# Kernel tuning notes

Hardware: AMD Instinct MI355X
Metric: run time of the kernel (lower is better)

Reference implementation:

```python
import jax, jax.numpy as jnp
import numpy as np

D_MODEL = 1024
D_FF = 2048
NUM_GROUPS = 4
EXPERTS_PER_GROUP = 4
TOP_K = 2
N_TOKENS = 4096
TOTAL_EXPERTS = NUM_GROUPS * EXPERTS_PER_GROUP


def setup_inputs() -> dict:
    key = jax.random.key(0)
    ks = jax.random.split(key, 7)
    s = 0.02
    return {
        "x": jax.random.normal(ks[0], (N_TOKENS, D_MODEL), dtype=jnp.float32),
        "Wg": jax.random.normal(ks[1], (D_MODEL, NUM_GROUPS), dtype=jnp.float32) * s,
        "We": jax.random.normal(ks[2], (D_MODEL, TOTAL_EXPERTS), dtype=jnp.float32) * s,
        "w1": jax.random.normal(ks[3], (TOTAL_EXPERTS, D_MODEL, D_FF), dtype=jnp.float32) * s,
        "b1": jnp.zeros((TOTAL_EXPERTS, D_FF), dtype=jnp.float32),
        "w2": jax.random.normal(ks[4], (TOTAL_EXPERTS, D_FF, D_MODEL), dtype=jnp.float32) * s,
        "b2": jnp.zeros((TOTAL_EXPERTS, D_MODEL), dtype=jnp.float32),
    }


def _router(x, Wg, We):
    N = x.shape[0]
    G, Eg = NUM_GROUPS, EXPERTS_PER_GROUP
    # Level 1: group gate
    group_probs = jax.nn.softmax(x @ Wg, axis=-1)            # [N, G]
    group_mask = group_probs >= (1.0 / G)
    # Level 2: expert gate (per-group softmax)
    expert_logits = (x @ We).reshape(N, G, Eg)
    expert_probs = jax.nn.softmax(expert_logits, axis=-1)    # [N, G, Eg]
    expert_mask = expert_probs >= (1.0 / Eg)
    valid_mask = (group_mask[:, :, None] & expert_mask).reshape(N, G * Eg)
    final_probs = (group_probs[:, :, None] * expert_probs).reshape(N, G * Eg)
    # Fallback: if fewer than top_k experts pass thresholds, use top-k by prob
    num_selected = valid_mask.sum(axis=-1)
    _, topk_idx = jax.lax.top_k(final_probs, TOP_K)          # [N, top_k]
    topk_mask = jnp.zeros((N, G * Eg), dtype=bool).at[
        jnp.arange(N)[:, None], topk_idx].set(True)
    use_topk = num_selected < TOP_K
    final_mask = jnp.where(use_topk[:, None], topk_mask, valid_mask)
    sel = final_probs * final_mask.astype(final_probs.dtype)
    w = sel / jnp.clip(sel.sum(axis=-1, keepdims=True), 1e-9)
    return final_mask, w                                      # [N, E], [N, E]


def reference(x, Wg, We, w1, b1, w2, b2):
    _, weights = _router(x, Wg, We)                          # [N, E]
    # Dense expert compute; masked-out experts contribute weight 0,
    # matching the gather/FFN/index_add loop in the original.
    h = jax.nn.gelu(jnp.einsum("nd,edf->nef", x, w1) + b1, approximate=False)
    y = jnp.einsum("nef,efd->ned", h, w2) + b2               # [N, E, D]
    return jnp.einsum("ne,ned->nd", weights, y)              # [N, D]
```

## Files before the change

kernel.cpp:

```cpp
#include <hip/hip_runtime.h>
#include <math.h>

#define NT 4096
#define DM 1024
#define DF 2048
#define NEXP 16

typedef __attribute__((ext_vector_type(8))) short bf16x8;
typedef __attribute__((ext_vector_type(4))) float f32x4;

__device__ __forceinline__ unsigned short f2bf(float f) {
  unsigned int u = __builtin_bit_cast(unsigned int, f);
  u += 0x7fffu + ((u >> 16) & 1u);
  return (unsigned short)(u >> 16);
}
__device__ __forceinline__ float bf2f(unsigned short s) {
  unsigned int u = ((unsigned int)s) << 16;
  return __builtin_bit_cast(float, u);
}

__device__ __forceinline__ void gload_lds16(const void* g, void* l) {
  __builtin_amdgcn_global_load_lds(
      (__attribute__((address_space(1))) void*)g,
      (__attribute__((address_space(3))) void*)l, 16, 0, 0);
}

__device__ __forceinline__ float gelu_f(float v) {
  float u = v * (0.7978845608f + 0.0356774081f * v * v);
  float t = 1.0f - 2.0f / (__expf(2.0f * u) + 1.0f);
  return 0.5f * v * (1.0f + t);
}

__device__ __forceinline__ void softmax4(float* v) {
  float m = fmaxf(fmaxf(v[0], v[1]), fmaxf(v[2], v[3]));
  float s = 0.f;
#pragma unroll
  for (int j = 0; j < 4; ++j) { v[j] = expf(v[j] - m); s += v[j]; }
  float inv = 1.f / s;
#pragma unroll
  for (int j = 0; j < 4; ++j) v[j] *= inv;
}

__global__ __launch_bounds__(256) void router2_kernel(
    const float* __restrict__ x, const float* __restrict__ Wg,
    const float* __restrict__ We, unsigned int* __restrict__ emask,
    float* __restrict__ eweight, unsigned short* __restrict__ xb) {
  int n = blockIdx.x;
  int tid = threadIdx.x;
  int c0 = tid * 4;
  float4 xv = *(const float4*)(x + (size_t)n * DM + c0);
  if (xb) {
    ushort4 o = make_ushort4(f2bf(xv.x), f2bf(xv.y), f2bf(xv.z), f2bf(xv.w));
    *(ushort4*)(xb + (size_t)n * DM + c0) = o;
  }
  float xa[4] = {xv.x, xv.y, xv.z, xv.w};
  float acc[20];
#pragma unroll
  for (int j = 0; j < 20; ++j) acc[j] = 0.f;
#pragma unroll
  for (int j = 0; j < 4; ++j) {
    int c = c0 + j;
    float4 wg = *(const float4*)(Wg + c * 4);
    acc[0] += xa[j] * wg.x; acc[1] += xa[j] * wg.y;
    acc[2] += xa[j] * wg.z; acc[3] += xa[j] * wg.w;
#pragma unroll
    for (int q = 0; q < 4; ++q) {
      float4 we = *(const float4*)(We + c * 16 + q * 4);
      acc[4 + q * 4 + 0] += xa[j] * we.x;
      acc[4 + q * 4 + 1] += xa[j] * we.y;
      acc[4 + q * 4 + 2] += xa[j] * we.z;
      acc[4 + q * 4 + 3] += xa[j] * we.w;
    }
  }
#pragma unroll
  for (int j = 0; j < 20; ++j) {
    float v = acc[j];
#pragma unroll
    for (int s = 32; s; s >>= 1) v += __shfl_xor(v, s, 64);
    acc[j] = v;
  }
  __shared__ float red[4][20];
  int lane = tid & 63, wv = tid >> 6;
  if (lane == 0) {
#pragma unroll
    for (int j = 0; j < 20; ++j) red[wv][j] = acc[j];
  }
  __syncthreads();
  if (tid == 0) {
    float t[20];
#pragma unroll
    for (int j = 0; j < 20; ++j)
      t[j] = red[0][j] + red[1][j] + red[2][j] + red[3][j];
    float gp[4] = {t[0], t[1], t[2], t[3]};
    softmax4(gp);
    float ep[16];
#pragma unroll
    for (int g = 0; g < 4; ++g) {
      float tt[4] = {t[4 + g * 4], t[5 + g * 4], t[6 + g * 4], t[7 + g * 4]};
      softmax4(tt);
#pragma unroll
      for (int i = 0; i < 4; ++i) ep[g * 4 + i] = tt[i];
    }
    float fp[16];
    bool valid[16];
    int nsel = 0;
#pragma unroll
    for (int g = 0; g < 4; ++g) {
      bool gm = gp[g] >= 0.25f;
#pragma unroll
      for (int i = 0; i < 4; ++i) {
        int e = g * 4 + i;
        bool em = ep[e] >= 0.25f;
        valid[e] = gm && em;
        fp[e] = gp[g] * ep[e];
        nsel += valid[e] ? 1 : 0;
      }
    }
    int m1 = 0; float v1 = -1.f;
#pragma unroll
    for (int e = 0; e < 16; ++e) if (fp[e] > v1) { v1 = fp[e]; m1 = e; }
    int m2 = -1; float v2 = -2.f;
#pragma unroll
    for (int e = 0; e < 16; ++e) if (e != m1 && fp[e] > v2) { v2 = fp[e]; m2 = e; }
    bool use_topk = nsel < 2;
    float sel[16]; float s = 0.f;
#pragma unroll
    for (int e = 0; e < 16; ++e) {
      bool msk = use_topk ? (e == m1 || e == m2) : valid[e];
      sel[e] = msk ? fp[e] : 0.f;
      s += sel[e];
      valid[e] = msk;
    }
    float inv = 1.f / fmaxf(s, 1e-9f);
    unsigned int mbits = 0;
    float wv16[16];
#pragma unroll
    for (int e = 0; e < 16; ++e) {
      mbits |= (valid[e] ? 1u : 0u) << e;
      wv16[e] = valid[e] ? sel[e] * inv : 0.f;
    }
    emask[n] = mbits;
#pragma unroll
    for (int i = 0; i < 4; ++i)
      *(float4*)(eweight + (size_t)n * 16 + i * 4) =
          make_float4(wv16[i * 4], wv16[i * 4 + 1], wv16[i * 4 + 2], wv16[i * 4 + 3]);
  }
}

__global__ __launch_bounds__(256) void compact_kernel(
    const unsigned int* __restrict__ emask, const float* __restrict__ eweight,
    int* __restrict__ counts, int* __restrict__ lists, float* __restrict__ wl,
    int* __restrict__ slotpos) {
  int e = blockIdx.x;
  int tid = threadIdx.x, lane = tid & 63, wv = tid >> 6;
  __shared__ int wcnt[4];
  int running = 0;
  for (int base = 0; base < NT; base += 256) {
    int n = base + tid;
    bool p = (emask[n] >> e) & 1u;
    unsigned long long bal = __ballot(p);
    int cnt = __popcll(bal);
    if (lane == 0) wcnt[wv] = cnt;
    __syncthreads();
    int off = running;
#pragma unroll
    for (int w = 0; w < 4; ++w)
      if (w < wv) off += wcnt[w];
    int tot = wcnt[0] + wcnt[1] + wcnt[2] + wcnt[3];
    if (p) {
      int pos = off + (int)__popcll(bal & ((1ull << lane) - 1ull));
      lists[e * NT + pos] = n;
      wl[e * NT + pos] = eweight[(size_t)n * 16 + e];
      slotpos[e * NT + n] = pos;
    }
    running += tot;
    __syncthreads();
  }
  if (tid == 0) counts[e] = running;
}

__global__ void prefix_kernel(const int* __restrict__ counts, int* __restrict__ base,
                              int* __restrict__ ent, int* __restrict__ nent) {
  if (threadIdx.x == 0 && blockIdx.x == 0) {
    int acc = 0, n = 0;
    for (int e = 0; e < NEXP; ++e) {
      base[e] = acc;
      acc += (counts[e] + 255) & ~255;
      int mt = (counts[e] + 127) >> 7;
      for (int m = 0; m < mt; ++m) ent[n++] = (e << 16) | m;
    }
    *nent = n;
  }
}

__global__ __launch_bounds__(256) void wtrans_kernel(
    const float* __restrict__ in, unsigned short* __restrict__ outp, int K, int N) {
  int e = blockIdx.z;
  int n0 = blockIdx.x * 64;
  int k0 = blockIdx.y * 64;
  const float* src = in + (size_t)e * K * N;
  unsigned short* dst = outp + (size_t)e * K * N;
  __shared__ unsigned short t[64][65];
  int tid = threadIdx.x;
#pragma unroll
  for (int it = 0; it < 4; ++it) {
    int idx = it * 256 + tid;
    int r = idx >> 4, c4 = (idx & 15) << 2;
    float4 v = *(const float4*)(src + (size_t)(k0 + r) * N + n0 + c4);
    t[r][c4 + 0] = f2bf(v.x);
    t[r][c4 + 1] = f2bf(v.y);
    t[r][c4 + 2] = f2bf(v.z);
    t[r][c4 + 3] = f2bf(v.w);
  }
  __syncthreads();
#pragma unroll
  for (int it = 0; it < 4; ++it) {
    int idx = it * 256 + tid;
    int r = idx >> 4, c4 = (idx & 15) << 2;
    ushort4 o;
    o.x = t[c4 + 0][r]; o.y = t[c4 + 1][r];
    o.z = t[c4 + 2][r]; o.w = t[c4 + 3][r];
    *(ushort4*)(dst + (size_t)(n0 + r) * K + k0 + c4) = o;
  }
}


__global__ __launch_bounds__(256, 4) void ffn1s_kernel(
    const unsigned short* __restrict__ xb, const unsigned short* __restrict__ wt,
    const float* __restrict__ b1, const int* __restrict__ counts,
    const int* __restrict__ lists, const int* __restrict__ base,
    unsigned short* __restrict__ h, int cap) {
  const int NN = DF / 128;
  const int NSLOT = 128;
  int b = blockIdx.x;
  int xcd = b & 7, slot = b >> 3;
  int e0 = xcd, e1 = xcd + 8;
  int c0 = counts[e0], c1 = counts[e1];
  int mt0 = (c0 + 127) >> 7, mt1 = (c1 + 127) >> 7;
  int T0 = mt0 * NN, T = T0 + mt1 * NN;

  __shared__ unsigned short lA[128 * 64];
  __shared__ unsigned short lB[128 * 64];

  int tid = threadIdx.x, lane = tid & 63, wid = tid >> 6;
  int wm = wid >> 1, wn = wid & 1;
  int lrow = lane & 15, lk = lane >> 4;
  int chunk = lane & 7, row_l = lane >> 3;

  for (int k = slot; k < T; k += NSLOT) {
    int e, mti, nt, count;
    if (k < T0) { e = e0; nt = k / mt0; mti = k % mt0; count = c0; }
    else        { int kk = k - T0; e = e1; nt = kk / mt1; mti = kk % mt1; count = c1; }
    int m0 = mti * 128, n0 = nt * 128;
    int hbase = base[e];
    if (hbase + m0 + 128 > cap) continue;
    const unsigned short* we = wt + (size_t)e * DM * DF;
    const int* lst = lists + e * NT + m0;

    const char* asrc[4];
    const char* bsrc[4];
#pragma unroll
    for (int c = 0; c < 4; ++c) {
      int r = wid * 32 + c * 8 + row_l;
      int sc = chunk ^ (r & 7);
      int rr = (m0 + r < count) ? r : 0;
      int tok = lst[rr];
      asrc[c] = (const char*)xb + (size_t)tok * DM * 2 + sc * 16;
      bsrc[c] = (const char*)we + (size_t)(n0 + r) * DM * 2 + sc * 16;
    }

    f32x4 acc[4][4];
#pragma unroll
    for (int m = 0; m < 4; ++m)
#pragma unroll
      for (int n = 0; n < 4; ++n) acc[m][n] = (f32x4)0.0f;

    for (int kt = 0; kt < DM / 64; ++kt) {
      __syncthreads();
#pragma unroll
      for (int c = 0; c < 4; ++c) {
        gload_lds16(asrc[c] + kt * 128, (void*)(lA + (wid * 32 + c * 8) * 64));
        gload_lds16(bsrc[c] + kt * 128, (void*)(lB + (wid * 32 + c * 8) * 64));
      }
      __syncthreads();
#pragma unroll
      for (int ks = 0; ks < 2; ++ks) {
        bf16x8 af[4], bfr[4];
#pragma unroll
        for (int m = 0; m < 4; ++m) {
          int row = wm * 64 + m * 16 + lrow;
          int off = row * 128 + (((ks * 64) + lk * 16) ^ ((row & 7) << 4));
          af[m] = *(const bf16x8*)((const char*)lA + off);
        }
#pragma unroll
        for (int n = 0; n < 4; ++n) {
          int row = wn * 64 + n * 16 + lrow;
          int off = row * 128 + (((ks * 64) + lk * 16) ^ ((row & 7) << 4));
          bfr[n] = *(const bf16x8*)((const char*)lB + off);
        }
#pragma unroll
        for (int m = 0; m < 4; ++m)
#pragma unroll
          for (int n = 0; n < 4; ++n)
            acc[m][n] = __builtin_amdgcn_mfma_f32_16x16x32_bf16(af[m], bfr[n], acc[m][n], 0, 0, 0);
      }
    }
#pragma unroll
    for (int m = 0; m < 4; ++m) {
      int rbase = hbase + m0 + wm * 64 + m * 16 + lk * 4;
#pragma unroll
      for (int n = 0; n < 4; ++n) {
        int col = n0 + wn * 64 + n * 16 + lrow;
        float bias = b1[e * DF + col];
#pragma unroll
        for (int j = 0; j < 4; ++j) {
          float v = acc[m][n][j] + bias;
          h[(size_t)(rbase + j) * DF + col] = f2bf(gelu_f(v));
        }
      }
    }
  }
}

__global__ __launch_bounds__(256, 4) void ffn2y_kernel(
    const unsigned short* __restrict__ h, const unsigned short* __restrict__ wt,
    const int* __restrict__ counts, const int* __restrict__ base,
    unsigned short* __restrict__ y, int cap) {
  const int NN = DM / 128;
  const int NSLOT = 128;
  int b = blockIdx.x;
  int xcd = b & 7, slot = b >> 3;
  int e0 = xcd, e1 = xcd + 8;
  int c0 = counts[e0], c1 = counts[e1];
  int mt0 = (c0 + 127) >> 7, mt1 = (c1 + 127) >> 7;
  int T0 = mt0 * NN, T = T0 + mt1 * NN;

  __shared__ unsigned short lA[128 * 64];
  __shared__ unsigned short lB[128 * 64];

  int tid = threadIdx.x, lane = tid & 63, wid = tid >> 6;
  int wm = wid >> 1, wn = wid & 1;
  int lrow = lane & 15, lk = lane >> 4;
  int chunk = lane & 7, row_l = lane >> 3;

  for (int k = slot; k < T; k += NSLOT) {
    int e, mti, nt, count;
    if (k < T0) { e = e0; nt = k / mt0; mti = k % mt0; count = c0; }
    else        { int kk = k - T0; e = e1; nt = kk / mt1; mti = kk % mt1; count = c1; }
    int m0 = mti * 128, n0 = nt * 128;
    int hbase = base[e];
    if (hbase + m0 + 128 > cap) continue;
    const unsigned short* we = wt + (size_t)e * DM * DF;

    const char* asrc[4];
    const char* bsrc[4];
#pragma unroll
    for (int c = 0; c < 4; ++c) {
      int r = wid * 32 + c * 8 + row_l;
      int sc = chunk ^ (r & 7);
      asrc[c] = (const char*)h + (size_t)(hbase + m0 + r) * DF * 2 + sc * 16;
      bsrc[c] = (const char*)we + (size_t)(n0 + r) * DF * 2 + sc * 16;
    }

    f32x4 acc[4][4];
#pragma unroll
    for (int m = 0; m < 4; ++m)
#pragma unroll
      for (int n = 0; n < 4; ++n) acc[m][n] = (f32x4)0.0f;

    for (int kt = 0; kt < DF / 64; ++kt) {
      __syncthreads();
#pragma unroll
      for (int c = 0; c < 4; ++c) {
        gload_lds16(asrc[c] + kt * 128, (void*)(lA + (wid * 32 + c * 8) * 64));
        gload_lds16(bsrc[c] + kt * 128, (void*)(lB + (wid * 32 + c * 8) * 64));
      }
      __syncthreads();
#pragma unroll
      for (int ks = 0; ks < 2; ++ks) {
        bf16x8 af[4], bfr[4];
#pragma unroll
        for (int m = 0; m < 4; ++m) {
          int row = wm * 64 + m * 16 + lrow;
          int off = row * 128 + (((ks * 64) + lk * 16) ^ ((row & 7) << 4));
          af[m] = *(const bf16x8*)((const char*)lA + off);
        }
#pragma unroll
        for (int n = 0; n < 4; ++n) {
          int row = wn * 64 + n * 16 + lrow;
          int off = row * 128 + (((ks * 64) + lk * 16) ^ ((row & 7) << 4));
          bfr[n] = *(const bf16x8*)((const char*)lB + off);
        }
#pragma unroll
        for (int m = 0; m < 4; ++m)
#pragma unroll
          for (int n = 0; n < 4; ++n)
            acc[m][n] = __builtin_amdgcn_mfma_f32_16x16x32_bf16(af[m], bfr[n], acc[m][n], 0, 0, 0);
      }
    }
#pragma unroll
    for (int m = 0; m < 4; ++m) {
      int rbase = hbase + m0 + wm * 64 + m * 16 + lk * 4;
      int lcl = m0 + wm * 64 + m * 16 + lk * 4;
#pragma unroll
      for (int n = 0; n < 4; ++n) {
        int col = n0 + wn * 64 + n * 16 + lrow;
#pragma unroll
        for (int j = 0; j < 4; ++j) {
          if (lcl + j < count)
            y[(size_t)(rbase + j) * DM + col] = f2bf(acc[m][n][j]);
        }
      }
    }
  }
}

__global__ __launch_bounds__(256) void reduce_kernel(
    const unsigned int* __restrict__ emask, const float* __restrict__ eweight,
    const int* __restrict__ slotpos, const int* __restrict__ base,
    const unsigned short* __restrict__ y, const float* __restrict__ b2,
    float* __restrict__ out) {
  int n = blockIdx.x;
  int tid = threadIdx.x;
  int c = tid * 4;
  unsigned int mask = emask[n];
  float4 accv = make_float4(0.f, 0.f, 0.f, 0.f);
  while (mask) {
    int e = __ffs(mask) - 1;
    mask &= mask - 1;
    float w = eweight[(size_t)n * 16 + e];
    int row = base[e] + slotpos[e * NT + n];
    ushort4 yv = *(const ushort4*)(y + (size_t)row * DM + c);
    float4 bv = *(const float4*)(b2 + e * DM + c);
    accv.x += w * (bf2f(yv.x) + bv.x);
    accv.y += w * (bf2f(yv.y) + bv.y);
    accv.z += w * (bf2f(yv.z) + bv.z);
    accv.w += w * (bf2f(yv.w) + bv.w);
  }
  *(float4*)(out + (size_t)n * DM + c) = accv;
}

__global__ __launch_bounds__(256, 4) void ffn2s_kernel(
    const unsigned short* __restrict__ h, const unsigned short* __restrict__ wt,
    const float* __restrict__ b2, const int* __restrict__ counts,
    const int* __restrict__ lists, const int* __restrict__ base,
    const float* __restrict__ wl, float* __restrict__ out, int cap) {
  const int NN = DM / 128;
  const int NSLOT = 128;
  int b = blockIdx.x;
  int xcd = b & 7, slot = b >> 3;
  int e0 = xcd, e1 = xcd + 8;
  int c0 = counts[e0], c1 = counts[e1];
  int mt0 = (c0 + 127) >> 7, mt1 = (c1 + 127) >> 7;
  int T0 = mt0 * NN, T = T0 + mt1 * NN;

  __shared__ unsigned short lA[128 * 64];
  __shared__ unsigned short lB[128 * 64];

  int tid = threadIdx.x, lane = tid & 63, wid = tid >> 6;
  int wm = wid >> 1, wn = wid & 1;
  int lrow = lane & 15, lk = lane >> 4;
  int chunk = lane & 7, row_l = lane >> 3;

  for (int k = slot; k < T; k += NSLOT) {
    int e, mti, nt, count;
    if (k < T0) { e = e0; nt = k / mt0; mti = k % mt0; count = c0; }
    else        { int kk = k - T0; e = e1; nt = kk / mt1; mti = kk % mt1; count = c1; }
    int m0 = mti * 128, n0 = nt * 128;
    int hbase = base[e];
    if (hbase + m0 + 128 > cap) continue;
    const unsigned short* we = wt + (size_t)e * DM * DF;

    const char* asrc[4];
    const char* bsrc[4];
#pragma unroll
    for (int c = 0; c < 4; ++c) {
      int r = wid * 32 + c * 8 + row_l;
      int sc = chunk ^ (r & 7);
      asrc[c] = (const char*)h + (size_t)(hbase + m0 + r) * DF * 2 + sc * 16;
      bsrc[c] = (const char*)we + (size_t)(n0 + r) * DF * 2 + sc * 16;
    }

    f32x4 acc[4][4];
#pragma unroll
    for (int m = 0; m < 4; ++m)
#pragma unroll
      for (int n = 0; n < 4; ++n) acc[m][n] = (f32x4)0.0f;

    for (int kt = 0; kt < DF / 64; ++kt) {
      __syncthreads();
#pragma unroll
      for (int c = 0; c < 4; ++c) {
        gload_lds16(asrc[c] + kt * 128, (void*)(lA + (wid * 32 + c * 8) * 64));
        gload_lds16(bsrc[c] + kt * 128, (void*)(lB + (wid * 32 + c * 8) * 64));
      }
      __syncthreads();
#pragma unroll
      for (int ks = 0; ks < 2; ++ks) {
        bf16x8 af[4], bfr[4];
#pragma unroll
        for (int m = 0; m < 4; ++m) {
          int row = wm * 64 + m * 16 + lrow;
          int off = row * 128 + (((ks * 64) + lk * 16) ^ ((row & 7) << 4));
          af[m] = *(const bf16x8*)((const char*)lA + off);
        }
#pragma unroll
        for (int n = 0; n < 4; ++n) {
          int row = wn * 64 + n * 16 + lrow;
          int off = row * 128 + (((ks * 64) + lk * 16) ^ ((row & 7) << 4));
          bfr[n] = *(const bf16x8*)((const char*)lB + off);
        }
#pragma unroll
        for (int m = 0; m < 4; ++m)
#pragma unroll
          for (int n = 0; n < 4; ++n)
            acc[m][n] = __builtin_amdgcn_mfma_f32_16x16x32_bf16(af[m], bfr[n], acc[m][n], 0, 0, 0);
      }
    }
#pragma unroll
    for (int m = 0; m < 4; ++m) {
      int rbase = m0 + wm * 64 + m * 16 + lk * 4;
#pragma unroll
      for (int n = 0; n < 4; ++n) {
        int col = n0 + wn * 64 + n * 16 + lrow;
        float bias = b2[e * DM + col];
#pragma unroll
        for (int j = 0; j < 4; ++j) {
          int sl = rbase + j;
          if (sl < count) {
            int tok = lists[e * NT + sl];
            float w = wl[e * NT + sl];
            atomicAdd(out + (size_t)tok * DM + col, w * (acc[m][n][j] + bias));
          }
        }
      }
    }
  }
}

__global__ __launch_bounds__(256) void ffn1_kernel(
    const float* __restrict__ x, const float* __restrict__ w1,
    const float* __restrict__ b1, const int* __restrict__ counts,
    const int* __restrict__ lists, const int* __restrict__ base,
    unsigned short* __restrict__ h, int cap, int e_arg) {
  int e = (e_arg >= 0) ? e_arg : (int)blockIdx.z;
  int count = counts[e];
  int m0 = blockIdx.y * 128;
  if (m0 >= count) return;
  int hbase = base[e];
  if (hbase + m0 + 128 > cap) return;
  int n0 = blockIdx.x * 128;
  const float* w1e = w1 + (size_t)e * DM * DF;
  const int* lst = lists + e * NT + m0;
  __shared__ unsigned short lA[128 * 64];
  __shared__ unsigned short lB[128 * 64];
  int tid = threadIdx.x;
  int lane = tid & 63, wid = tid >> 6;
  int wm = wid >> 1, wn = wid & 1;
  int lrow = lane & 15, lk = lane >> 4;
  f32x4 acc[4][4];
#pragma unroll
  for (int m = 0; m < 4; ++m)
#pragma unroll
    for (int n = 0; n < 4; ++n) acc[m][n] = (f32x4)0.0f;
  for (int kt = 0; kt < DM / 64; ++kt) {
    int k0 = kt * 64;
    __syncthreads();
#pragma unroll
    for (int p = 0; p < 8; ++p) {
      int idx = p * 256 + tid;
      int r = idx >> 4, c4 = idx & 15;
      int tok = (m0 + r < count) ? lst[r] : lst[0];
      float4 v = *(const float4*)(x + (size_t)tok * DM + k0 + c4 * 4);
      ushort4 bv = make_ushort4(f2bf(v.x), f2bf(v.y), f2bf(v.z), f2bf(v.w));
      int off = r * 128 + ((c4 * 8) ^ ((r & 7) << 4));
      *(ushort4*)((char*)lA + off) = bv;
    }
#pragma unroll
    for (int p = 0; p < 16; ++p) {
      int idx = p * 256 + tid;
      int n = idx & 127, k2 = idx >> 7;
      const float* bp = w1e + (size_t)(k0 + 2 * k2) * DF + n0 + n;
      ushort2 bv = make_ushort2(f2bf(bp[0]), f2bf(bp[DF]));
      int off = n * 128 + ((k2 * 4) ^ ((n & 7) << 4));
      *(ushort2*)((char*)lB + off) = bv;
    }
    __syncthreads();
#pragma unroll
    for (int ks = 0; ks < 2; ++ks) {
      bf16x8 af[4], bfr[4];
#pragma unroll
      for (int m = 0; m < 4; ++m) {
        int row = wm * 64 + m * 16 + lrow;
        int off = row * 128 + (((ks * 64) + lk * 16) ^ ((row & 7) << 4));
        af[m] = *(const bf16x8*)((const char*)lA + off);
      }
#pragma unroll
      for (int n = 0; n < 4; ++n) {
        int row = wn * 64 + n * 16 + lrow;
        int off = row * 128 + (((ks * 64) + lk * 16) ^ ((row & 7) << 4));
        bfr[n] = *(const bf16x8*)((const char*)lB + off);
      }
#pragma unroll
      for (int m = 0; m < 4; ++m)
#pragma unroll
        for (int n = 0; n < 4; ++n)
          acc[m][n] = __builtin_amdgcn_mfma_f32_16x16x32_bf16(af[m], bfr[n], acc[m][n], 0, 0, 0);
    }
  }
#pragma unroll
  for (int m = 0; m < 4; ++m) {
    int rbase = hbase + m0 + wm * 64 + m * 16 + lk * 4;
#pragma unroll
    for (int n = 0; n < 4; ++n) {
      int col = n0 + wn * 64 + n * 16 + lrow;
      float bias = b1[e * DF + col];
#pragma unroll
      for (int j = 0; j < 4; ++j) {
        float v = acc[m][n][j] + bias;
        h[(size_t)(rbase + j) * DF + col] = f2bf(gelu_f(v));
      }
    }
  }
}

__global__ __launch_bounds__(256) void ffn2_kernel(
    const unsigned short* __restrict__ h, const float* __restrict__ w2,
    const float* __restrict__ b2, const int* __restrict__ counts,
    const int* __restrict__ lists, const int* __restrict__ base,
    const float* __restrict__ wl, float* __restrict__ out, int cap, int e_arg) {
  int e = (e_arg >= 0) ? e_arg : (int)blockIdx.z;
  int count = counts[e];
  int m0 = blockIdx.y * 128;
  if (m0 >= count) return;
  int hbase = base[e];
  if (hbase + m0 + 128 > cap) return;
  int n0 = blockIdx.x * 128;
  const float* w2e = w2 + (size_t)e * DF * DM;
  __shared__ unsigned short lA[128 * 64];
  __shared__ unsigned short lB[128 * 64];
  int tid = threadIdx.x;
  int lane = tid & 63, wid = tid >> 6;
  int wm = wid >> 1, wn = wid & 1;
  int lrow = lane & 15, lk = lane >> 4;
  f32x4 acc[4][4];
#pragma unroll
  for (int m = 0; m < 4; ++m)
#pragma unroll
    for (int n = 0; n < 4; ++n) acc[m][n] = (f32x4)0.0f;
  for (int kt = 0; kt < DF / 64; ++kt) {
    int k0 = kt * 64;
    __syncthreads();
#pragma unroll
    for (int p = 0; p < 8; ++p) {
      int idx = p * 256 + tid;
      int r = idx >> 4, c4 = idx & 15;
      ushort4 v = *(const ushort4*)(h + (size_t)(hbase + m0 + r) * DF + k0 + c4 * 4);
      int off = r * 128 + ((c4 * 8) ^ ((r & 7) << 4));
      *(ushort4*)((char*)lA + off) = v;
    }
#pragma unroll
    for (int p = 0; p < 16; ++p) {
      int idx = p * 256 + tid;
      int n = idx & 127, k2 = idx >> 7;
      const float* bp = w2e + (size_t)(k0 + 2 * k2) * DM + n0 + n;
      ushort2 bv = make_ushort2(f2bf(bp[0]), f2bf(bp[DM]));
      int off = n * 128 + ((k2 * 4) ^ ((n & 7) << 4));
      *(ushort2*)((char*)lB + off) = bv;
    }
    __syncthreads();
#pragma unroll
    for (int ks = 0; ks < 2; ++ks) {
      bf16x8 af[4], bfr[4];
#pragma unroll
      for (int m = 0; m < 4; ++m) {
        int row = wm * 64 + m * 16 + lrow;
        int off = row * 128 + (((ks * 64) + lk * 16) ^ ((row & 7) << 4));
        af[m] = *(const bf16x8*)((const char*)lA + off);
      }
#pragma unroll
      for (int n = 0; n < 4; ++n) {
        int row = wn * 64 + n * 16 + lrow;
        int off = row * 128 + (((ks * 64) + lk * 16) ^ ((row & 7) << 4));
        bfr[n] = *(const bf16x8*)((const char*)lB + off);
      }
#pragma unroll
      for (int m = 0; m < 4; ++m)
#pragma unroll
        for (int n = 0; n < 4; ++n)
          acc[m][n] = __builtin_amdgcn_mfma_f32_16x16x32_bf16(af[m], bfr[n], acc[m][n], 0, 0, 0);
    }
  }
#pragma unroll
  for (int m = 0; m < 4; ++m) {
    int rbase = m0 + wm * 64 + m * 16 + lk * 4;
#pragma unroll
    for (int n = 0; n < 4; ++n) {
      int col = n0 + wn * 64 + n * 16 + lrow;
      float bias = b2[e * DM + col];
#pragma unroll
      for (int j = 0; j < 4; ++j) {
        int slot = rbase + j;
        if (slot < count) {
          int tok = lists[e * NT + slot];
          float w = wl[e * NT + slot];
          atomicAdd(out + (size_t)tok * DM + col, w * (acc[m][n][j] + bias));
        }
      }
    }
  }
}

extern "C" void kernel_launch(void* const* d_in, const int* in_sizes, int n_in,
                              void* d_out, int out_size, void* d_ws, size_t ws_size,
                              hipStream_t stream) {
  const float* x  = (const float*)d_in[0];
  const float* Wg = (const float*)d_in[1];
  const float* We = (const float*)d_in[2];
  const float* w1 = (const float*)d_in[3];
  const float* b1 = (const float*)d_in[4];
  const float* w2 = (const float*)d_in[5];
  const float* b2 = (const float*)d_in[6];
  float* out = (float*)d_out;

  char* ws = (char*)d_ws;
  int* counts = (int*)ws;
  int* base   = (int*)(ws + 256);
  int* nent   = (int*)(ws + 576);
  int* ent    = (int*)(ws + 1024);
  unsigned int* emask = (unsigned int*)(ws + 4096);
  int* lists  = (int*)(ws + 32768);
  float* wl   = (float*)(ws + 32768 + NEXP * NT * 4);
  float* eweight = (float*)(ws + 32768 + 2 * NEXP * NT * 4);
  int* slotpos   = (int*)(ws + 32768 + 3 * NEXP * NT * 4);

  const size_t OFF_XB = 2u << 20;
  const size_t OFF_WT = OFF_XB + ((size_t)NT * DM * 2);
  const size_t OFF_H  = OFF_WT + ((size_t)NEXP * DM * DF * 2);
  long cap6 = ((long)ws_size - (long)OFF_H) / (DF * 2 + DM * 2);
  long cap4 = ((long)ws_size - (long)OFF_H) / (DF * 2);
  bool fast = (cap4 >= 20000);

  unsigned short* xb_router = fast ? (unsigned short*)(ws + OFF_XB) : (unsigned short*)0;

  hipMemsetAsync(out, 0, (size_t)NT * DM * sizeof(float), stream);
  hipMemsetAsync(ws, 0, 1024, stream);
  router2_kernel<<<NT, 256, 0, stream>>>(x, Wg, We, emask, eweight, xb_router);
  compact_kernel<<<NEXP, 256, 0, stream>>>(emask, eweight, counts, lists, wl, slotpos);

  if (fast) {
    unsigned short* xb = (unsigned short*)(ws + OFF_XB);
    unsigned short* wt = (unsigned short*)(ws + OFF_WT);
    unsigned short* h  = (unsigned short*)(ws + OFF_H);
    prefix_kernel<<<1, 64, 0, stream>>>(counts, base, ent, nent);
    wtrans_kernel<<<dim3(DF / 64, DM / 64, NEXP), 256, 0, stream>>>(w1, wt, DM, DF);
    if (cap6 >= 20000) {
      int cap = (int)(cap6 > 65536 ? 65536 : cap6);
      unsigned short* y = (unsigned short*)(ws + OFF_H + (size_t)cap * DF * 2);
      ffn1s_kernel<<<1024, 256, 0, stream>>>(xb, wt, b1, counts, lists, base, h, cap);
      wtrans_kernel<<<dim3(DM / 64, DF / 64, NEXP), 256, 0, stream>>>(w2, wt, DF, DM);
      ffn2y_kernel<<<1024, 256, 0, stream>>>(h, wt, counts, base, y, cap);
      reduce_kernel<<<NT, 256, 0, stream>>>(emask, eweight, slotpos, base, y, b2, out);
    } else {
      int cap = (int)(cap4 > 65536 ? 65536 : cap4);
      ffn1s_kernel<<<1024, 256, 0, stream>>>(xb, wt, b1, counts, lists, base, h, cap);
      wtrans_kernel<<<dim3(DM / 64, DF / 64, NEXP), 256, 0, stream>>>(w2, wt, DF, DM);
      ffn2s_kernel<<<1024, 256, 0, stream>>>(h, wt, b2, counts, lists, base, wl, out, cap);
    }
  } else {
    unsigned short* h = (unsigned short*)(ws + OFF_XB);
    long cap_rows = ((long)ws_size - (long)OFF_XB) / (DF * 2);
    if (cap_rows >= 24576) {
      int cap = (int)(cap_rows > 65536 ? 65536 : cap_rows);
      prefix_kernel<<<1, 64, 0, stream>>>(counts, base, ent, nent);
      ffn1_kernel<<<dim3(DF / 128, NT / 128, NEXP), 256, 0, stream>>>(
          x, w1, b1, counts, lists, base, h, cap, -1);
      ffn2_kernel<<<dim3(DM / 128, NT / 128, NEXP), 256, 0, stream>>>(
          h, w2, b2, counts, lists, base, wl, out, cap, -1);
    } else {
      hipMemsetAsync(base, 0, 64, stream);
      for (int e = 0; e < NEXP; ++e) {
        ffn1_kernel<<<dim3(DF / 128, NT / 128, 1), 256, 0, stream>>>(
            x, w1, b1, counts, lists, base, h, NT, e);
        ffn2_kernel<<<dim3(DM / 128, NT / 128, 1), 256, 0, stream>>>(
            h, w2, b2, counts, lists, base, wl, out, NT, e);
      }
    }
  }
}
```

Baseline: 310.6 us.

## Fuse weight transposes into router and FFN1 kernels via extra blocks

Adds dedicated blocks to the router kernel that transpose and convert w1 to bf16 while other blocks compute routing, and adds blocks to the FFN1 kernel that transpose w2 into a separate buffer while FFN1 runs. This removes the standalone wtrans launches and their serialization, so conversion overlaps with compute. It needs extra workspace for a separate w2t buffer and falls back to the old sequence when workspace is short. The fallback small path now calls prefix_kernel after the base memset, which may change behavior there.

Result: no change. 314.2 us (+1.2%).

```diff
diff --git a/kernel.cpp b/kernel.cpp
--- a/kernel.cpp
+++ b/kernel.cpp
@@ -41,12 +41,52 @@
   for (int j = 0; j < 4; ++j) v[j] *= inv;
 }
 
-__global__ __launch_bounds__(256) void router2_kernel(
+__device__ __forceinline__ void trans_tile(
+    const float* __restrict__ src, unsigned short* __restrict__ dst,
+    int K, int N, int k0, int n0, unsigned short (*t)[65], int tid) {
+#pragma unroll
+  for (int it = 0; it < 4; ++it) {
+    int idx = it * 256 + tid;
+    int r = idx >> 4, c4 = (idx & 15) << 2;
+    float4 v = *(const float4*)(src + (size_t)(k0 + r) * N + n0 + c4);
+    t[r][c4 + 0] = f2bf(v.x);
+    t[r][c4 + 1] = f2bf(v.y);
+    t[r][c4 + 2] = f2bf(v.z);
+    t[r][c4 + 3] = f2bf(v.w);
+  }
+  __syncthreads();
+#pragma unroll
+  for (int it = 0; it < 4; ++it) {
+    int idx = it * 256 + tid;
+    int r = idx >> 4, c4 = (idx & 15) << 2;
+    ushort4 o;
+    o.x = t[c4 + 0][r]; o.y = t[c4 + 1][r];
+    o.z = t[c4 + 2][r]; o.w = t[c4 + 3][r];
+    *(ushort4*)(dst + (size_t)(n0 + r) * K + k0 + c4) = o;
+  }
+  __syncthreads();
+}
+
+__global__ __launch_bounds__(256) void prep1_kernel(
     const float* __restrict__ x, const float* __restrict__ Wg,
     const float* __restrict__ We, unsigned int* __restrict__ emask,
-    float* __restrict__ eweight, unsigned short* __restrict__ xb) {
-  int n = blockIdx.x;
-  int tid = threadIdx.x;
+    float* __restrict__ eweight, unsigned short* __restrict__ xb,
+    const float* __restrict__ w1, unsigned short* __restrict__ w1t, int wtB) {
+  __shared__ unsigned short tbuf[64][65];
+  __shared__ float red[4][20];
+  int id = blockIdx.x, tid = threadIdx.x;
+  if (id < wtB) {
+    int per = 8192 / wtB;
+    for (int i = 0; i < per; ++i) {
+      int t = id * per + i;
+      int e = t >> 9, rem = t & 511;
+      int n0 = (rem & 31) * 64, k0 = (rem >> 5) * 64;
+      trans_tile(w1 + (size_t)e * DM * DF, w1t + (size_t)e * DM * DF,
+                 DM, DF, k0, n0, tbuf, tid);
+    }
+    return;
+  }
+  int n = id - wtB;
   int c0 = tid * 4;
   float4 xv = *(const float4*)(x + (size_t)n * DM + c0);
   if (xb) {
@@ -79,7 +119,6 @@
     for (int s = 32; s; s >>= 1) v += __shfl_xor(v, s, 64);
     acc[j] = v;
   }
-  __shared__ float red[4][20];
   int lane = tid & 63, wv = tid >> 6;
   if (lane == 0) {
 #pragma unroll
@@ -195,54 +234,45 @@
 
 __global__ __launch_bounds__(256) void wtrans_kernel(
     const float* __restrict__ in, unsigned short* __restrict__ outp, int K, int N) {
+  __shared__ unsigned short t[64][65];
   int e = blockIdx.z;
   int n0 = blockIdx.x * 64;
   int k0 = blockIdx.y * 64;
-  const float* src = in + (size_t)e * K * N;
-  unsigned short* dst = outp + (size_t)e * K * N;
-  __shared__ unsigned short t[64][65];
-  int tid = threadIdx.x;
-#pragma unroll
-  for (int it = 0; it < 4; ++it) {
-    int idx = it * 256 + tid;
-    int r = idx >> 4, c4 = (idx & 15) << 2;
-    float4 v = *(const float4*)(src + (size_t)(k0 + r) * N + n0 + c4);
-    t[r][c4 + 0] = f2bf(v.x);
-    t[r][c4 + 1] = f2bf(v.y);
-    t[r][c4 + 2] = f2bf(v.z);
-    t[r][c4 + 3] = f2bf(v.w);
-  }
-  __syncthreads();
-#pragma unroll
-  for (int it = 0; it < 4; ++it) {
-    int idx = it * 256 + tid;
-    int r = idx >> 4, c4 = (idx & 15) << 2;
-    ushort4 o;
-    o.x = t[c4 + 0][r]; o.y = t[c4 + 1][r];
-    o.z = t[c4 + 2][r]; o.w = t[c4 + 3][r];
-    *(ushort4*)(dst + (size_t)(n0 + r) * K + k0 + c4) = o;
-  }
-}
-
-
-__global__ __launch_bounds__(256, 4) void ffn1s_kernel(
+  trans_tile(in + (size_t)e * K * N, outp + (size_t)e * K * N, K, N, k0, n0, t,
+             threadIdx.x);
+}
+
+__global__ __launch_bounds__(256, 4) void ffn1h_kernel(
     const unsigned short* __restrict__ xb, const unsigned short* __restrict__ wt,
     const float* __restrict__ b1, const int* __restrict__ counts,
     const int* __restrict__ lists, const int* __restrict__ base,
-    unsigned short* __restrict__ h, int cap) {
+    unsigned short* __restrict__ h, int cap,
+    const float* __restrict__ w2, unsigned short* __restrict__ w2t, int wtB) {
+  __shared__ unsigned short lA[128 * 64];
+  __shared__ unsigned short lB[128 * 64];
+  int id = blockIdx.x, tid = threadIdx.x;
+  if (id < wtB) {
+    unsigned short(*tbuf)[65] = (unsigned short(*)[65])lA;
+    int per = 8192 / wtB;
+    for (int i = 0; i < per; ++i) {
+      int t = id * per + i;
+      int e = t >> 9, rem = t & 511;
+      int n0 = (rem & 15) * 64, k0 = (rem >> 4) * 64;
+      trans_tile(w2 + (size_t)e * DF * DM, w2t + (size_t)e * DF * DM,
+                 DF, DM, k0, n0, tbuf, tid);
+    }
+    return;
+  }
+  int g = id - wtB;
   const int NN = DF / 128;
   const int NSLOT = 128;
-  int b = blockIdx.x;
-  int xcd = b & 7, slot = b >> 3;
+  int xcd = g & 7, slot = g >> 3;
   int e0 = xcd, e1 = xcd + 8;
   int c0 = counts[e0], c1 = counts[e1];
   int mt0 = (c0 + 127) >> 7, mt1 = (c1 + 127) >> 7;
   int T0 = mt0 * NN, T = T0 + mt1 * NN;
 
-  __shared__ unsigned short lA[128 * 64];
-  __shared__ unsigned short lB[128 * 64];
-
-  int tid = threadIdx.x, lane = tid & 63, wid = tid >> 6;
+  int lane = tid & 63, wid = tid >> 6;
   int wm = wid >> 1, wn = wid & 1;
   int lrow = lane & 15, lk = lane >> 4;
   int chunk = lane & 7, row_l = lane >> 3;
@@ -734,40 +764,62 @@
   float* eweight = (float*)(ws + 32768 + 2 * NEXP * NT * 4);
   int* slotpos   = (int*)(ws + 32768 + 3 * NEXP * NT * 4);
 
-  const size_t OFF_XB = 2u << 20;
-  const size_t OFF_WT = OFF_XB + ((size_t)NT * DM * 2);
-  const size_t OFF_H  = OFF_WT + ((size_t)NEXP * DM * DF * 2);
-  long cap6 = ((long)ws_size - (long)OFF_H) / (DF * 2 + DM * 2);
-  long cap4 = ((long)ws_size - (long)OFF_H) / (DF * 2);
-  bool fast = (cap4 >= 20000);
-
-  unsigned short* xb_router = fast ? (unsigned short*)(ws + OFF_XB) : (unsigned short*)0;
+  const size_t OFF_XB  = (size_t)2 << 20;
+  const size_t OFF_W1T = OFF_XB + ((size_t)NT * DM * 2);
+  const size_t WTSZ    = (size_t)NEXP * DM * DF * 2;
+  const size_t OFF_W2T = OFF_W1T + WTSZ;
+  const size_t OFF_H_A = OFF_W2T + WTSZ;
+  const size_t OFF_H_B = OFF_W1T + WTSZ;
+
+  long capA = ((long)ws_size - (long)OFF_H_A) / ((DF + DM) * 2);
+  long capB = ((long)ws_size - (long)OFF_H_B) / ((DF + DM) * 2);
+  long capC = ((long)ws_size - (long)OFF_H_B) / (DF * 2);
+  bool fast = (capC >= 20000);
+
+  unsigned short* xb = (unsigned short*)(ws + OFF_XB);
+  unsigned short* w1t = (unsigned short*)(ws + OFF_W1T);
 
   hipMemsetAsync(out, 0, (size_t)NT * DM * sizeof(float), stream);
   hipMemsetAsync(ws, 0, 1024, stream);
-  router2_kernel<<<NT, 256, 0, stream>>>(x, Wg, We, emask, eweight, xb_router);
-  compact_kernel<<<NEXP, 256, 0, stream>>>(emask, eweight, counts, lists, wl, slotpos);
 
   if (fast) {
-    unsigned short* xb = (unsigned short*)(ws + OFF_XB);
-    unsigned short* wt = (unsigned short*)(ws + OFF_WT);
-    unsigned short* h  = (unsigned short*)(ws + OFF_H);
+    prep1_kernel<<<1024 + NT, 256, 0, stream>>>(x, Wg, We, emask, eweight, xb,
+                                                w1, w1t, 1024);
+    compact_kernel<<<NEXP, 256, 0, stream>>>(emask, eweight, counts, lists, wl, slotpos);
     prefix_kernel<<<1, 64, 0, stream>>>(counts, base, ent, nent);
-    wtrans_kernel<<<dim3(DF / 64, DM / 64, NEXP), 256, 0, stream>>>(w1, wt, DM, DF);
-    if (cap6 >= 20000) {
-      int cap = (int)(cap6 > 65536 ? 65536 : cap6);
-      unsigned short* y = (unsigned short*)(ws + OFF_H + (size_t)cap * DF * 2);
-      ffn1s_kernel<<<1024, 256, 0, stream>>>(xb, wt, b1, counts, lists, base, h, cap);
-      wtrans_kernel<<<dim3(DM / 64, DF / 64, NEXP), 256, 0, stream>>>(w2, wt, DF, DM);
-      ffn2y_kernel<<<1024, 256, 0, stream>>>(h, wt, counts, base, y, cap);
+
+    if (capA >= 20000) {
+      int cap = (int)(capA > 65536 ? 65536 : capA);
+      unsigned short* w2t = (unsigned short*)(ws + OFF_W2T);
+      unsigned short* h = (unsigned short*)(ws + OFF_H_A);
+      unsigned short* y = (unsigned short*)(ws + OFF_H_A + (size_t)cap * DF * 2);
+      ffn1h_kernel<<<512 + 1024, 256, 0, stream>>>(
+          xb, w1t, b1, counts, lists, base, h, cap, w2, w2t, 512);
+      ffn2y_kernel<<<1024, 256, 0, stream>>>(h, w2t, counts, base, y, cap);
+      reduce_kernel<<<NT, 256, 0, stream>>>(emask, eweight, slotpos, base, y, b2, out);
+    } else if (capB >= 20000) {
+      int cap = (int)(capB > 65536 ? 65536 : capB);
+      unsigned short* h = (unsigned short*)(ws + OFF_H_B);
+      unsigned short* y = (unsigned short*)(ws + OFF_H_B + (size_t)cap * DF * 2);
+      ffn1h_kernel<<<1024, 256, 0, stream>>>(
+          xb, w1t, b1, counts, lists, base, h, cap, (const float*)0,
+          (unsigned short*)0, 0);
+      wtrans_kernel<<<dim3(DM / 64, DF / 64, NEXP), 256, 0, stream>>>(w2, w1t, DF, DM);
+      ffn2y_kernel<<<1024, 256, 0, stream>>>(h, w1t, counts, base, y, cap);
       reduce_kernel<<<NT, 256, 0, stream>>>(emask, eweight, slotpos, base, y, b2, out);
     } else {
-      int cap = (int)(cap4 > 65536 ? 65536 : cap4);
-      ffn1s_kernel<<<1024, 256, 0, stream>>>(xb, wt, b1, counts, lists, base, h, cap);
-      wtrans_kernel<<<dim3(DM / 64, DF / 64, NEXP), 256, 0, stream>>>(w2, wt, DF, DM);
-      ffn2s_kernel<<<1024, 256, 0, stream>>>(h, wt, b2, counts, lists, base, wl, out, cap);
+      int cap = (int)(capC > 65536 ? 65536 : capC);
+      unsigned short* h = (unsigned short*)(ws + OFF_H_B);
+      ffn1h_kernel<<<1024, 256, 0, stream>>>(
+          xb, w1t, b1, counts, lists, base, h, cap, (const float*)0,
+          (unsigned short*)0, 0);
+      wtrans_kernel<<<dim3(DM / 64, DF / 64, NEXP), 256, 0, stream>>>(w2, w1t, DF, DM);
+      ffn2s_kernel<<<1024, 256, 0, stream>>>(h, w1t, b2, counts, lists, base, wl, out, cap);
     }
   } else {
+    prep1_kernel<<<NT, 256, 0, stream>>>(x, Wg, We, emask, eweight,
+                                         (unsigned short*)0, w1, w1t, 0);
+    compact_kernel<<<NEXP, 256, 0, stream>>>(emask, eweight, counts, lists, wl, slotpos);
     unsigned short* h = (unsigned short*)(ws + OFF_XB);
     long cap_rows = ((long)ws_size - (long)OFF_XB) / (DF * 2);
     if (cap_rows >= 24576) {
@@ -779,6 +831,7 @@
           h, w2, b2, counts, lists, base, wl, out, cap, -1);
     } else {
       hipMemsetAsync(base, 0, 64, stream);
+      prefix_kernel<<<1, 64, 0, stream>>>(counts, base, ent, nent);
       for (int e = 0; e < NEXP; ++e) {
         ffn1_kernel<<<dim3(DF / 128, NT / 128, 1), 256, 0, stream>>>(
             x, w1, b1, counts, lists, base, h, NT, e);
```
